# Optimization experiments

Measured on AMD Instinct MI355X. Metric: run time of the kernel, lower is better.

The kernel has to match this reference:

```python
import jax, jax.numpy as jnp
import numpy as np

B, T, H, IN = 256, 1024, 512, 1

def setup_inputs() -> dict:
    key = jax.random.key(0)
    ks = jax.random.split(key, 10)
    s = 1.0 / np.sqrt(H)
    return {
        "input": jax.random.normal(ks[0], (B, T), dtype=jnp.float32),
        "Wx0": jax.random.uniform(ks[1], (IN, 4 * H), jnp.float32, -s, s),
        "Wh0": jax.random.uniform(ks[2], (H, 4 * H), jnp.float32, -s, s),
        "b0": jax.random.uniform(ks[3], (4 * H,), jnp.float32, -s, s),
        "Wx1": jax.random.uniform(ks[4], (H, 4 * H), jnp.float32, -s, s),
        "Wh1": jax.random.uniform(ks[5], (H, 4 * H), jnp.float32, -s, s),
        "b1": jax.random.uniform(ks[6], (4 * H,), jnp.float32, -s, s),
        "Wf": jax.random.uniform(ks[7], (H, 1), jnp.float32, -s, s),
        "bf": jax.random.uniform(ks[8], (1,), jnp.float32, -s, s),
    }

def _lstm_layer(xs, Wx, Wh, b):
    # xs: [T, B, in] -> hs: [T, B, H]
    Bd = xs.shape[1]
    Hd = Wh.shape[0]
    h0 = jnp.zeros((Bd, Hd), xs.dtype)
    c0 = jnp.zeros((Bd, Hd), xs.dtype)
    def step(carry, x_t):
        h, c = carry
        g = x_t @ Wx + h @ Wh + b                     # [B, 4H]
        i, f, gg, o = jnp.split(g, 4, axis=-1)
        i = jax.nn.sigmoid(i)
        f = jax.nn.sigmoid(f)
        gg = jnp.tanh(gg)
        o = jax.nn.sigmoid(o)
        c_n = f * c + i * gg
        h_n = o * jnp.tanh(c_n)
        return (h_n, c_n), h_n
    _, hs = jax.lax.scan(step, (h0, c0), xs)
    return hs

def reference(input, Wx0, Wh0, b0, Wx1, Wh1, b1, Wf, bf):
    # input: [B, T] scalar sequence (input_size = 1)
    xs = input.T[:, :, None]                           # [T, B, 1]
    h1 = _lstm_layer(xs, Wx0, Wh0, b0)                 # [T, B, H]
    h2 = _lstm_layer(h1, Wx1, Wh1, b1)                 # [T, B, H]
    out = h2 @ Wf + bf                                 # [T, B, 1]
    return out[:, :, 0].T                              # [B, T]
```

## Files before the change

### kernel.cpp

```cpp
#include <hip/hip_runtime.h>


typedef _Float16 f16;
typedef _Float16 f16x8 __attribute__((ext_vector_type(8)));
typedef float f32x4 __attribute__((ext_vector_type(4)));
typedef unsigned long long u64;

#define NB 256
#define NT_ 1024
#define NH 512
#define RING 16
#define SLOT (NB * NH)

__device__ __forceinline__ float sigm(float x)  { return 1.0f / (1.0f + __expf(-x)); }
__device__ __forceinline__ float tanhx(float x) { return 2.0f / (1.0f + __expf(-2.0f * x)) - 1.0f; }

__device__ __forceinline__ void st8(unsigned short* p, u64 v) {
  __hip_atomic_store((u64*)p, v, __ATOMIC_RELAXED, __HIP_MEMORY_SCOPE_AGENT);
}
__device__ __forceinline__ void stf(unsigned* p, unsigned v) {
  __hip_atomic_store(p, v, __ATOMIC_RELAXED, __HIP_MEMORY_SCOPE_AGENT);
}
__device__ __forceinline__ unsigned ldf(const unsigned* p) {
  return __hip_atomic_load(p, __ATOMIC_RELAXED, __HIP_MEMORY_SCOPE_AGENT);
}
__device__ __forceinline__ unsigned pollr(const unsigned* a, unsigned thr) {
  unsigned v;
  for (;;) {
    v = ldf(a);
    if (!~__ballot(v >= thr)) break;
    __builtin_amdgcn_s_sleep(1);
  }
  asm volatile("" ::: "memory");
  return v;
}

__device__ __forceinline__ unsigned* PFL(unsigned* pf, int c, int j, int r) {
  return pf + (((c * 32 + j) * 4) + r) * 32;
}
__device__ __forceinline__ unsigned* QFL(unsigned* qf, int c, int j, int r) {
  return qf + (((c * 32 + j) * 4) + r) * 32;
}

__global__ void prep_xT(const float* __restrict__ inp, float* __restrict__ xT) {
  int g = blockIdx.x * 256 + threadIdx.x;
  int t = g >> 8, b = g & 255;
  xT[t * NB + b] = inp[b * NT_ + t];
}

__global__ void prep_w(const float* __restrict__ Wh0,
                       const float* __restrict__ Wx1,
                       const float* __restrict__ Wh1,
                       f16* __restrict__ dst) {
  int g = blockIdx.x * 256 + threadIdx.x;
  int mat = g >> 20;
  int r = g & 0xFFFFF;
  int j = r & 7, ln = (r >> 3) & 63, kt = (r >> 9) & 15;
  int cl = ln & 15, qd = ln >> 4;
  int k = kt * 32 + qd * 8 + j;
  int jt = (r >> 13) & 1, nh = (r >> 14) & 1, sl = (r >> 15) & 31;
  const float* W = (mat == 0) ? Wh0 : (mat == 1) ? Wx1 : Wh1;
  int gate = jt * 2 + (cl >> 3);
  int gcol = gate * 512 + sl * 16 + nh * 8 + (cl & 7);
  size_t di = (size_t)mat * 1048576 + (size_t)sl * 32768 +
              (((size_t)(nh * 2 + jt) * 16 + kt) * 64 + ln) * 8 + j;
  dst[di] = (f16)W[(size_t)k * 2048 + gcol];
}

__global__ void reduce_out(const float* __restrict__ part8,
                           const float* __restrict__ bfp,
                           float* __restrict__ out) {
  int g = blockIdx.x * 256 + threadIdx.x;
  float v = bfp[0];
#pragma unroll
  for (int j = 0; j < 8; ++j) v += part8[(size_t)j * (NB * NT_) + g];
  out[g] = v;
}

__global__ __launch_bounds__(256, 1) void lstm_main(
    const float* __restrict__ xT,
    const f16*  __restrict__ wsl,
    const float* __restrict__ wx0,
    const float* __restrict__ bias0,
    const float* __restrict__ bias1,
    const float* __restrict__ wf,
    unsigned short* p_hi, unsigned short* p_lo,
    unsigned short* q_hi, unsigned short* q_lo,
    unsigned int* pf,
    unsigned int* qf,
    float* part8)
{
  extern __shared__ char smem[];
  const int tid = threadIdx.x;
  const int wv = tid >> 6, ln = tid & 63;
  const int qd = ln >> 4, cl = ln & 15;
  const int bx = blockIdx.x;
  const int r8 = bx & 7, idx = bx >> 3;
  const bool isL0 = !(r8 & 1);
  const int c = r8 >> 1;
  const int sl = idx;
  const float LO = 1.0f / 1024.0f;
  const int u = cl & 7, g01 = cl >> 3;
  const bool hiH = (cl < 8);
  const int lr = wv * 16 + cl;

  if (isL0) {
    const int4* s0 = (const int4*)wsl + (size_t)sl * 4096;
    int4* d = (int4*)smem;
    for (int i = tid; i < 4096; i += 256) d[i] = s0[i];
  } else {
    const int4* s1 = (const int4*)wsl + 131072 + (size_t)sl * 4096;
    const int4* s2 = (const int4*)wsl + 262144 + (size_t)sl * 4096;
    int4* d = (int4*)smem;
    for (int i = tid; i < 4096; i += 256) { d[i] = s1[i]; d[4096 + i] = s2[i]; }
  }
  __syncthreads();

  if (isL0) {
    float w0a[2], w0b[2], b0a[2], b0b[2];
#pragma unroll
    for (int nh = 0; nh < 2; ++nh) {
      int base = sl * 16 + nh * 8 + u;
      w0a[nh] = wx0[g01 * 512 + base];
      b0a[nh] = bias0[g01 * 512 + base];
      w0b[nh] = wx0[(2 + g01) * 512 + base];
      b0b[nh] = bias0[(2 + g01) * 512 + base];
    }
    float cst[2][4] = {{0.f,0.f,0.f,0.f},{0.f,0.f,0.f,0.f}};
    const unsigned* pwa = (ln < 32) ? PFL(pf, c, ln, sl & 3)
                                    : QFL(qf, c, ln - 32, sl & 3);
    const f16x8* wl = (const f16x8*)smem;
    f16* sh  = (f16*)(smem + 65536);
    f16* slo = sh + 1024;

    for (int s = 0; s < NT_; ++s) {
      if ((s & (RING - 1)) == 0 && s) {
        __syncthreads();
        if (wv == 0)
          asm volatile("buffer_inv sc1\n\ts_waitcnt vmcnt(0)" ::: "memory");
        __syncthreads();
      }
      const int slot_r = (s + RING - 1) & (RING - 1);
      const int slot_w = s & (RING - 1);
      float4 xv = *(const float4*)(xT + s * NB + c * 64 + wv * 16 + qd * 4);
      if (s) {
        unsigned thr = (ln < 32) ? (unsigned)s
                                 : (s >= RING ? (unsigned)(s - RING + 1) : 0u);
        pollr(pwa, thr);
      }
      const f16* ah = (const f16*)p_hi + (size_t)slot_r * SLOT + (size_t)c * 32768 +
                      (qd >> 1) * 1024 + lr * 16 + (qd & 1) * 8;
      const f16* al = (const f16*)p_lo + (size_t)slot_r * SLOT + (size_t)c * 32768 +
                      (qd >> 1) * 1024 + lr * 16 + (qd & 1) * 8;
      f16x8 Ah[16], Al[16];
#pragma unroll
      for (int kt = 0; kt < 16; ++kt) {
        Ah[kt] = *(const f16x8*)(ah + kt * 2048);
        Al[kt] = *(const f16x8*)(al + kt * 2048);
      }
      f32x4 acc[4], accL[4];
#pragma unroll
      for (int t4 = 0; t4 < 4; ++t4) {
        acc[t4] = (f32x4){0.f,0.f,0.f,0.f};
        accL[t4] = (f32x4){0.f,0.f,0.f,0.f};
      }
#pragma unroll
      for (int kt = 0; kt < 16; ++kt) {
#pragma unroll
        for (int t4 = 0; t4 < 4; ++t4) {
          f16x8 bw = wl[(t4 * 16 + kt) * 64 + ln];
          acc[t4]  = __builtin_amdgcn_mfma_f32_16x16x32_f16(Ah[kt], bw, acc[t4], 0, 0, 0);
          accL[t4] = __builtin_amdgcn_mfma_f32_16x16x32_f16(Al[kt], bw, accL[t4], 0, 0, 0);
        }
      }
#pragma unroll
      for (int e = 0; e < 4; ++e) {
        float xe = (e == 0) ? xv.x : (e == 1) ? xv.y : (e == 2) ? xv.z : xv.w;
        int r = wv * 16 + qd * 4 + e;
#pragma unroll
        for (int nh = 0; nh < 2; ++nh) {
          float v0 = acc[nh*2+0][e] + accL[nh*2+0][e] * LO + xe * w0a[nh] + b0a[nh];
          float v1 = acc[nh*2+1][e] + accL[nh*2+1][e] * LO + xe * w0b[nh] + b0b[nh];
          float w0 = __shfl_xor(v0, 8, 16);
          float w1 = __shfl_xor(v1, 8, 16);
          float gi = hiH ? v0 : w0;
          float gf = hiH ? w0 : v0;
          float gg = hiH ? v1 : w1;
          float go = hiH ? w1 : v1;
          float ii = sigm(gi), ff = sigm(gf), tg = tanhx(gg), oo = sigm(go);
          cst[nh][e] = ff * cst[nh][e] + ii * tg;
          float h = oo * tanhx(cst[nh][e]);
          int su = r * 16 + nh * 8 + u;
          if (hiH) {
            sh[su] = (f16)h;
          } else {
            f16 hh = (f16)h;
            slo[su] = (f16)((h - (float)hh) * 1024.0f);
          }
        }
      }
      __syncthreads();
      {
        unsigned short* bh = p_hi + (size_t)slot_w * SLOT + (size_t)c * 32768 + (size_t)sl * 1024;
        unsigned short* bl = p_lo + (size_t)slot_w * SLOT + (size_t)c * 32768 + (size_t)sl * 1024;
#pragma unroll
        for (int i = tid; i < 512; i += 256) {
          int strm = i >> 8, pc = i & 255;
          const f16* src = (strm ? slo : sh) + pc * 4;
          st8((strm ? bl : bh) + pc * 4, *(const u64*)src);
        }
      }
      __syncthreads();
      if (tid < 4)
        stf(PFL(pf, c, sl, tid), (unsigned)(s + 1));
    }
  } else {
    float b1c0[2], b1c1[2], wfv[2];
#pragma unroll
    for (int nh = 0; nh < 2; ++nh) {
      int base = sl * 16 + nh * 8 + u;
      b1c0[nh] = bias1[g01 * 512 + base];
      b1c1[nh] = bias1[(2 + g01) * 512 + base];
      wfv[nh] = wf[base];
    }
    float cst[2][4] = {{0.f,0.f,0.f,0.f},{0.f,0.f,0.f,0.f}};
    const unsigned* a_init = (ln < 32) ? QFL(qf, c, ln, sl & 3)
                                       : PFL(pf, c, ln - 32, sl & 3);
    const unsigned* ppf = PFL(pf, c, ln & 31, (sl + (ln >> 5)) & 3);
    const f16x8* wx_ = (const f16x8*)smem;
    const f16x8* wh_ = (const f16x8*)(smem + 65536);
    f16* sh  = (f16*)(smem + 131072);
    f16* slo = sh + 1024;

    for (int s = 0; s < NT_; ++s) {
      if ((s & (RING - 1)) == 0 && s) {
        __syncthreads();
        if (wv == 0)
          asm volatile("buffer_inv sc1\n\ts_waitcnt vmcnt(0)" ::: "memory");
        __syncthreads();
      }
      const int slot_r = (s + RING - 1) & (RING - 1);
      const int slot_w = s & (RING - 1);
      bool early = false;
      if (s) {
        unsigned thr_i = (ln < 32) ? (unsigned)s : (unsigned)(s + 1);
        unsigned v = ldf(a_init);
        u64 bal = __ballot(v >= thr_i);
        while ((unsigned)bal != 0xFFFFFFFFu) {
          __builtin_amdgcn_s_sleep(1);
          v = ldf(a_init);
          bal = __ballot(v >= thr_i);
        }
        asm volatile("" ::: "memory");
        early = ((unsigned)(bal >> 32) == 0xFFFFFFFFu);
      }
      const f16* aqh = (const f16*)q_hi + (size_t)slot_r * SLOT + (size_t)c * 32768 +
                       (qd >> 1) * 1024 + lr * 16 + (qd & 1) * 8;
      const f16* aql = (const f16*)q_lo + (size_t)slot_r * SLOT + (size_t)c * 32768 +
                       (qd >> 1) * 1024 + lr * 16 + (qd & 1) * 8;
      f16x8 Aq[16][2];
#pragma unroll
      for (int kt = 0; kt < 16; ++kt) {
        Aq[kt][0] = *(const f16x8*)(aqh + kt * 2048);
        Aq[kt][1] = *(const f16x8*)(aql + kt * 2048);
      }
      const f16* aph = (const f16*)p_hi + (size_t)slot_w * SLOT + (size_t)c * 32768 +
                       (qd >> 1) * 1024 + lr * 16 + (qd & 1) * 8;
      const f16* apl = (const f16*)p_lo + (size_t)slot_w * SLOT + (size_t)c * 32768 +
                       (qd >> 1) * 1024 + lr * 16 + (qd & 1) * 8;
      f16x8 Ap[16][2];
      if (early) {
#pragma unroll
        for (int kt = 0; kt < 16; ++kt) {
          Ap[kt][0] = *(const f16x8*)(aph + kt * 2048);
          Ap[kt][1] = *(const f16x8*)(apl + kt * 2048);
        }
      }
      f32x4 acc[4], accL[4];
#pragma unroll
      for (int t4 = 0; t4 < 4; ++t4) {
        acc[t4] = (f32x4){0.f,0.f,0.f,0.f};
        accL[t4] = (f32x4){0.f,0.f,0.f,0.f};
      }
#pragma unroll
      for (int kt = 0; kt < 16; ++kt) {
#pragma unroll
        for (int t4 = 0; t4 < 4; ++t4) {
          f16x8 bw = wh_[(t4 * 16 + kt) * 64 + ln];
          acc[t4]  = __builtin_amdgcn_mfma_f32_16x16x32_f16(Aq[kt][0], bw, acc[t4], 0, 0, 0);
          accL[t4] = __builtin_amdgcn_mfma_f32_16x16x32_f16(Aq[kt][1], bw, accL[t4], 0, 0, 0);
        }
      }
      if (!early) {
        pollr(ppf, (unsigned)(s + 1));
#pragma unroll
        for (int kt = 0; kt < 16; ++kt) {
          Ap[kt][0] = *(const f16x8*)(aph + kt * 2048);
          Ap[kt][1] = *(const f16x8*)(apl + kt * 2048);
        }
      }
#pragma unroll
      for (int kt = 0; kt < 16; ++kt) {
#pragma unroll
        for (int t4 = 0; t4 < 4; ++t4) {
          f16x8 bw = wx_[(t4 * 16 + kt) * 64 + ln];
          acc[t4]  = __builtin_amdgcn_mfma_f32_16x16x32_f16(Ap[kt][0], bw, acc[t4], 0, 0, 0);
          accL[t4] = __builtin_amdgcn_mfma_f32_16x16x32_f16(Ap[kt][1], bw, accL[t4], 0, 0, 0);
        }
      }
      float po[4];
#pragma unroll
      for (int e = 0; e < 4; ++e) {
        po[e] = 0.0f;
#pragma unroll
        for (int nh = 0; nh < 2; ++nh) {
          float v0 = acc[nh*2+0][e] + accL[nh*2+0][e] * LO + b1c0[nh];
          float v1 = acc[nh*2+1][e] + accL[nh*2+1][e] * LO + b1c1[nh];
          float w0 = __shfl_xor(v0, 8, 16);
          float w1 = __shfl_xor(v1, 8, 16);
          float gi = hiH ? v0 : w0;
          float gf = hiH ? w0 : v0;
          float gg = hiH ? v1 : w1;
          float go = hiH ? w1 : v1;
          float ii = sigm(gi), ff = sigm(gf), tg = tanhx(gg), oo = sigm(go);
          cst[nh][e] = ff * cst[nh][e] + ii * tg;
          float h = oo * tanhx(cst[nh][e]);
          int su = (wv * 16 + qd * 4 + e) * 16 + nh * 8 + u;
          if (hiH) {
            sh[su] = (f16)h;
          } else {
            f16 hh = (f16)h;
            slo[su] = (f16)((h - (float)hh) * 1024.0f);
          }
          po[e] += hiH ? wfv[nh] * h : 0.0f;
        }
      }
      __syncthreads();
      {
        unsigned short* bhq = q_hi + (size_t)slot_w * SLOT + (size_t)c * 32768 + (size_t)sl * 1024;
        unsigned short* blq = q_lo + (size_t)slot_w * SLOT + (size_t)c * 32768 + (size_t)sl * 1024;
#pragma unroll
        for (int i = tid; i < 512; i += 256) {
          int strm = i >> 8, pc = i & 255;
          const f16* src = (strm ? slo : sh) + pc * 4;
          st8((strm ? blq : bhq) + pc * 4, *(const u64*)src);
        }
      }
      __syncthreads();
      if (tid < 4)
        stf(QFL(qf, c, sl, tid), (unsigned)(s + 1));
#pragma unroll
      for (int e = 0; e < 4; ++e) {
        float r = po[e];
#pragma unroll
        for (int m = 1; m < 16; m <<= 1) r += __shfl_xor(r, m, 16);
        if (cl == 0)
          atomicAdd(part8 + (size_t)(sl & 7) * (NB * NT_) +
                        (size_t)(c * 64 + wv * 16 + qd * 4 + e) * NT_ + s, r);
      }
    }
  }
}

extern "C" void kernel_launch(void* const* d_in, const int* in_sizes, int n_in,
                              void* d_out, int out_size, void* d_ws, size_t ws_size,
                              hipStream_t stream) {
  (void)in_sizes; (void)n_in; (void)out_size; (void)ws_size;
  const float* inp = (const float*)d_in[0];
  const float* Wx0 = (const float*)d_in[1];
  const float* Wh0 = (const float*)d_in[2];
  const float* b0  = (const float*)d_in[3];
  const float* Wx1 = (const float*)d_in[4];
  const float* Wh1 = (const float*)d_in[5];
  const float* b1  = (const float*)d_in[6];
  const float* Wf  = (const float*)d_in[7];
  const float* bf  = (const float*)d_in[8];

  const size_t MB = 1u << 20;
  const size_t OFF_W    = 0;
  const size_t OFF_XT   = 6 * MB;
  const size_t OFF_PHI  = 7 * MB;
  const size_t OFF_PLO  = 11 * MB;
  const size_t OFF_QHI  = 15 * MB;
  const size_t OFF_QLO  = 19 * MB;
  const size_t OFF_PART = 23 * MB;
  const size_t OFF_CTR  = 31 * MB;

  char* ws = (char*)d_ws;
  f16* wsl = (f16*)(ws + OFF_W);
  float* xT = (float*)(ws + OFF_XT);
  unsigned short* phi = (unsigned short*)(ws + OFF_PHI);
  unsigned short* plo = (unsigned short*)(ws + OFF_PLO);
  unsigned short* qhi = (unsigned short*)(ws + OFF_QHI);
  unsigned short* qlo = (unsigned short*)(ws + OFF_QLO);
  float* part8 = (float*)(ws + OFF_PART);
  unsigned int* pfl = (unsigned int*)(ws + OFF_CTR);
  unsigned int* qfl = pfl + 16384;
  float* out = (float*)d_out;

  (void)hipFuncSetAttribute((const void*)lstm_main,
                            hipFuncAttributeMaxDynamicSharedMemorySize, 135168);

  (void)hipMemsetAsync(ws + OFF_PHI, 0, (OFF_CTR + 131072) - OFF_PHI, stream);

  prep_xT<<<1024, 256, 0, stream>>>(inp, xT);
  prep_w<<<12288, 256, 0, stream>>>(Wh0, Wx1, Wh1, wsl);

  lstm_main<<<256, 256, 135168, stream>>>(xT, wsl, Wx0, b0, b1, Wf,
                                          phi, plo, qhi, qlo, pfl, qfl, part8);

  reduce_out<<<1024, 256, 0, stream>>>(part8, bf, out);
}
```

Before: 9.664 ms.

## Add XCC-local fast path for LSTM step exchange with L2-scope sync

At startup each block reads its XCC id. When all 32 blocks of a group share one XCC, the group takes a fast path that exchanges per-step hidden states through XCC-local ring buffers using plain volatile stores and loads, buffer_inv without sc1, and new local flags. Layer-1 blocks copy the layer-0 output from the global ring into a local import buffer, so the cross-layer handoff is decoupled from the local recurrence. The global ring shrinks to 8 slots. The aim is to avoid the cost of device-scope coherence on every recurrent step, at the price of extra copies, more flags, and dependence on the scheduler placing groups on the same XCC.

```diff
diff --git a/kernel.cpp b/kernel.cpp
--- a/kernel.cpp
+++ b/kernel.cpp
@@ -9,7 +9,8 @@
 #define NB 256
 #define NT_ 1024
 #define NH 512
-#define RING 16
+#define RING 8
+#define RL 4
 #define SLOT (NB * NH)
 
 __device__ __forceinline__ float sigm(float x)  { return 1.0f / (1.0f + __expf(-x)); }
@@ -23,6 +24,9 @@
 }
 __device__ __forceinline__ unsigned ldf(const unsigned* p) {
   return __hip_atomic_load(p, __ATOMIC_RELAXED, __HIP_MEMORY_SCOPE_AGENT);
+}
+__device__ __forceinline__ u64 ldf64(const unsigned short* p) {
+  return __hip_atomic_load((const u64*)p, __ATOMIC_RELAXED, __HIP_MEMORY_SCOPE_AGENT);
 }
 __device__ __forceinline__ unsigned pollr(const unsigned* a, unsigned thr) {
   unsigned v;
@@ -34,12 +38,26 @@
   asm volatile("" ::: "memory");
   return v;
 }
+__device__ __forceinline__ void stv32(unsigned* p, unsigned v) { *(volatile unsigned*)p = v; }
+__device__ __forceinline__ void stv64(unsigned short* p, u64 v) { *(volatile u64*)p = v; }
+__device__ __forceinline__ void pollv(const unsigned* a, unsigned thr) {
+  for (;;) {
+    unsigned v = *(volatile const unsigned*)a;
+    if (!~__ballot(v >= thr)) break;
+    __builtin_amdgcn_s_sleep(1);
+    asm volatile("buffer_inv" ::: "memory");
+  }
+  asm volatile("" ::: "memory");
+}
 
 __device__ __forceinline__ unsigned* PFL(unsigned* pf, int c, int j, int r) {
   return pf + (((c * 32 + j) * 4) + r) * 32;
 }
 __device__ __forceinline__ unsigned* QFL(unsigned* qf, int c, int j, int r) {
   return qf + (((c * 32 + j) * 4) + r) * 32;
+}
+__device__ __forceinline__ unsigned* LFL(unsigned* lf, int kind, int c, int j) {
+  return lf + (((kind * 4 + c) * 32) + j) * 32;
 }
 
 __global__ void prep_xT(const float* __restrict__ inp, float* __restrict__ xT) {
@@ -86,8 +104,12 @@
     const float* __restrict__ wf,
     unsigned short* p_hi, unsigned short* p_lo,
     unsigned short* q_hi, unsigned short* q_lo,
-    unsigned int* pf,
-    unsigned int* qf,
+    unsigned int* pf, unsigned int* qf,
+    unsigned short* ploc_hi, unsigned short* ploc_lo,
+    unsigned short* qloc_hi, unsigned short* qloc_lo,
+    unsigned short* pimp_hi, unsigned short* pimp_lo,
+    unsigned int* lf,
+    unsigned int* xtab,
     float* part8)
 {
   extern __shared__ char smem[];
@@ -114,6 +136,13 @@
     int4* d = (int4*)smem;
     for (int i = tid; i < 4096; i += 256) { d[i] = s1[i]; d[4096 + i] = s2[i]; }
   }
+
+  unsigned myx;
+  asm("s_getreg_b32 %0, hwreg(HW_REG_XCC_ID)" : "=s"(myx));
+  unsigned* xgrp = xtab + (isL0 ? 0 : 128) + c * 32;
+  if (tid == 0) stf(xgrp + sl, myx + 1);
+  unsigned xv_ = pollr(xgrp + (ln & 31), 1);
+  bool fast = __all((int)(xv_ == (unsigned)__shfl((int)xv_, 0)));
   __syncthreads();
 
   if (isL0) {
@@ -127,31 +156,54 @@
       b0b[nh] = bias0[(2 + g01) * 512 + base];
     }
     float cst[2][4] = {{0.f,0.f,0.f,0.f},{0.f,0.f,0.f,0.f}};
-    const unsigned* pwa = (ln < 32) ? PFL(pf, c, ln, sl & 3)
-                                    : QFL(qf, c, ln - 32, sl & 3);
     const f16x8* wl = (const f16x8*)smem;
     f16* sh  = (f16*)(smem + 65536);
     f16* slo = sh + 1024;
+    const unsigned* lpf = (const unsigned*)LFL(lf, 0, c, ln & 31);
+    const unsigned* agq = QFL(qf, c, ln & 31, sl & 3);
 
     for (int s = 0; s < NT_; ++s) {
-      if ((s & (RING - 1)) == 0 && s) {
-        __syncthreads();
-        if (wv == 0)
-          asm volatile("buffer_inv sc1\n\ts_waitcnt vmcnt(0)" ::: "memory");
-        __syncthreads();
-      }
-      const int slot_r = (s + RING - 1) & (RING - 1);
-      const int slot_w = s & (RING - 1);
+      const int inv_per = fast ? (RL - 1) : (RING - 1);
+      if ((s & inv_per) == 0 && s) {
+        __syncthreads();
+        if (wv == 0) {
+          if (fast) asm volatile("buffer_inv" ::: "memory");
+          else      asm volatile("buffer_inv sc1\n\ts_waitcnt vmcnt(0)" ::: "memory");
+        }
+        __syncthreads();
+      }
+      const int slw8 = s & (RING - 1);
       float4 xv = *(const float4*)(xT + s * NB + c * 64 + wv * 16 + qd * 4);
       if (s) {
-        unsigned thr = (ln < 32) ? (unsigned)s
-                                 : (s >= RING ? (unsigned)(s - RING + 1) : 0u);
-        pollr(pwa, thr);
-      }
-      const f16* ah = (const f16*)p_hi + (size_t)slot_r * SLOT + (size_t)c * 32768 +
-                      (qd >> 1) * 1024 + lr * 16 + (qd & 1) * 8;
-      const f16* al = (const f16*)p_lo + (size_t)slot_r * SLOT + (size_t)c * 32768 +
-                      (qd >> 1) * 1024 + lr * 16 + (qd & 1) * 8;
+        unsigned thrG = (s >= RING) ? (unsigned)(s - RING + 1) : 0u;
+        if (fast) {
+          for (;;) {
+            unsigned v = (ln < 32) ? *(volatile const unsigned*)lpf : ldf(agq);
+            unsigned t = (ln < 32) ? (unsigned)s : thrG;
+            if (!~__ballot(v >= t)) break;
+            __builtin_amdgcn_s_sleep(1);
+            asm volatile("buffer_inv" ::: "memory");
+          }
+          asm volatile("" ::: "memory");
+        } else {
+          const unsigned* pwa = (ln < 32) ? PFL(pf, c, ln, sl & 3) : agq;
+          pollr(pwa, (ln < 32) ? (unsigned)s : thrG);
+        }
+      }
+      const f16* ah; const f16* al;
+      if (fast) {
+        int slr = (s + RL - 1) & (RL - 1);
+        size_t b0_ = (size_t)(c * RL + slr) * 32768 +
+                     (qd >> 1) * 1024 + lr * 16 + (qd & 1) * 8;
+        ah = (const f16*)ploc_hi + b0_;
+        al = (const f16*)ploc_lo + b0_;
+      } else {
+        int slr8 = (s + RING - 1) & (RING - 1);
+        size_t b0_ = (size_t)slr8 * SLOT + (size_t)c * 32768 +
+                     (qd >> 1) * 1024 + lr * 16 + (qd & 1) * 8;
+        ah = (const f16*)p_hi + b0_;
+        al = (const f16*)p_lo + b0_;
+      }
       f16x8 Ah[16], Al[16];
 #pragma unroll
       for (int kt = 0; kt < 16; ++kt) {
@@ -200,19 +252,48 @@
         }
       }
       __syncthreads();
-      {
-        unsigned short* bh = p_hi + (size_t)slot_w * SLOT + (size_t)c * 32768 + (size_t)sl * 1024;
-        unsigned short* bl = p_lo + (size_t)slot_w * SLOT + (size_t)c * 32768 + (size_t)sl * 1024;
+      if (fast) {
+        if (s && tid < 4) stf(PFL(pf, c, sl, tid), (unsigned)s);
+        {
+          unsigned short* bh = ploc_hi + (size_t)(c * RL + (s & (RL - 1))) * 32768 + (size_t)sl * 1024;
+          unsigned short* bl = ploc_lo + (size_t)(c * RL + (s & (RL - 1))) * 32768 + (size_t)sl * 1024;
+#pragma unroll
+          for (int i = tid; i < 512; i += 256) {
+            int strm = i >> 8, pc = i & 255;
+            const f16* src = (strm ? slo : sh) + pc * 4;
+            stv64((strm ? bl : bh) + pc * 4, *(const u64*)src);
+          }
+        }
+        asm volatile("s_waitcnt vmcnt(0)" ::: "memory");
+        __syncthreads();
+        if (tid == 0) stv32(LFL(lf, 0, c, sl), (unsigned)(s + 1));
+        {
+          unsigned short* bh = p_hi + (size_t)slw8 * SLOT + (size_t)c * 32768 + (size_t)sl * 1024;
+          unsigned short* bl = p_lo + (size_t)slw8 * SLOT + (size_t)c * 32768 + (size_t)sl * 1024;
+#pragma unroll
+          for (int i = tid; i < 512; i += 256) {
+            int strm = i >> 8, pc = i & 255;
+            const f16* src = (strm ? slo : sh) + pc * 4;
+            st8((strm ? bl : bh) + pc * 4, *(const u64*)src);
+          }
+        }
+      } else {
+        unsigned short* bh = p_hi + (size_t)slw8 * SLOT + (size_t)c * 32768 + (size_t)sl * 1024;
+        unsigned short* bl = p_lo + (size_t)slw8 * SLOT + (size_t)c * 32768 + (size_t)sl * 1024;
 #pragma unroll
         for (int i = tid; i < 512; i += 256) {
           int strm = i >> 8, pc = i & 255;
           const f16* src = (strm ? slo : sh) + pc * 4;
           st8((strm ? bl : bh) + pc * 4, *(const u64*)src);
         }
-      }
+        __syncthreads();
+        if (tid < 4) stf(PFL(pf, c, sl, tid), (unsigned)(s + 1));
+      }
+    }
+    if (fast) {
+      asm volatile("s_waitcnt vmcnt(0)" ::: "memory");
       __syncthreads();
-      if (tid < 4)
-        stf(PFL(pf, c, sl, tid), (unsigned)(s + 1));
+      if (tid < 4) stf(PFL(pf, c, sl, tid), (unsigned)NT_);
     }
   } else {
     float b1c0[2], b1c1[2], wfv[2];
@@ -224,139 +305,255 @@
       wfv[nh] = wf[base];
     }
     float cst[2][4] = {{0.f,0.f,0.f,0.f},{0.f,0.f,0.f,0.f}};
-    const unsigned* a_init = (ln < 32) ? QFL(qf, c, ln, sl & 3)
-                                       : PFL(pf, c, ln - 32, sl & 3);
-    const unsigned* ppf = PFL(pf, c, ln & 31, (sl + (ln >> 5)) & 3);
     const f16x8* wx_ = (const f16x8*)smem;
     const f16x8* wh_ = (const f16x8*)(smem + 65536);
     f16* sh  = (f16*)(smem + 131072);
     f16* slo = sh + 1024;
+    const unsigned* lqf = (const unsigned*)LFL(lf, 1, c, ln & 31);
+    const unsigned* lif = (const unsigned*)LFL(lf, 2, c, ln & 31);
 
     for (int s = 0; s < NT_; ++s) {
-      if ((s & (RING - 1)) == 0 && s) {
-        __syncthreads();
-        if (wv == 0)
-          asm volatile("buffer_inv sc1\n\ts_waitcnt vmcnt(0)" ::: "memory");
-        __syncthreads();
-      }
-      const int slot_r = (s + RING - 1) & (RING - 1);
-      const int slot_w = s & (RING - 1);
-      bool early = false;
-      if (s) {
-        unsigned thr_i = (ln < 32) ? (unsigned)s : (unsigned)(s + 1);
-        unsigned v = ldf(a_init);
-        u64 bal = __ballot(v >= thr_i);
-        while ((unsigned)bal != 0xFFFFFFFFu) {
-          __builtin_amdgcn_s_sleep(1);
-          v = ldf(a_init);
-          bal = __ballot(v >= thr_i);
-        }
-        asm volatile("" ::: "memory");
-        early = ((unsigned)(bal >> 32) == 0xFFFFFFFFu);
-      }
-      const f16* aqh = (const f16*)q_hi + (size_t)slot_r * SLOT + (size_t)c * 32768 +
-                       (qd >> 1) * 1024 + lr * 16 + (qd & 1) * 8;
-      const f16* aql = (const f16*)q_lo + (size_t)slot_r * SLOT + (size_t)c * 32768 +
-                       (qd >> 1) * 1024 + lr * 16 + (qd & 1) * 8;
-      f16x8 Aq[16][2];
-#pragma unroll
-      for (int kt = 0; kt < 16; ++kt) {
-        Aq[kt][0] = *(const f16x8*)(aqh + kt * 2048);
-        Aq[kt][1] = *(const f16x8*)(aql + kt * 2048);
-      }
-      const f16* aph = (const f16*)p_hi + (size_t)slot_w * SLOT + (size_t)c * 32768 +
-                       (qd >> 1) * 1024 + lr * 16 + (qd & 1) * 8;
-      const f16* apl = (const f16*)p_lo + (size_t)slot_w * SLOT + (size_t)c * 32768 +
-                       (qd >> 1) * 1024 + lr * 16 + (qd & 1) * 8;
-      f16x8 Ap[16][2];
-      if (early) {
+      const int inv_per = fast ? (RL - 1) : (RING - 1);
+      if ((s & inv_per) == 0 && s) {
+        __syncthreads();
+        if (wv == 0) {
+          if (fast) asm volatile("buffer_inv" ::: "memory");
+          else      asm volatile("buffer_inv sc1\n\ts_waitcnt vmcnt(0)" ::: "memory");
+        }
+        __syncthreads();
+      }
+      const int slw8 = s & (RING - 1);
+      const int slw4 = s & (RL - 1);
+
+      if (fast) {
+        if (s) pollv(lqf, (unsigned)s);
+        pollr(PFL(pf, c, sl, ln & 3), (unsigned)(s + 1));
+        {
+          size_t so = (size_t)slw8 * SLOT + (size_t)c * 32768 + (size_t)sl * 1024 + tid * 4;
+          size_t dof = (size_t)(c * RL + slw4) * 32768 + (size_t)sl * 1024 + tid * 4;
+          u64 vh = ldf64(p_hi + so);
+          u64 vl = ldf64(p_lo + so);
+          stv64(pimp_hi + dof, vh);
+          stv64(pimp_lo + dof, vl);
+        }
+        asm volatile("s_waitcnt vmcnt(0)" ::: "memory");
+        __syncthreads();
+        if (tid == 0) stv32(LFL(lf, 2, c, sl), (unsigned)(s + 1));
+        size_t qb = (size_t)(c * RL + ((s + RL - 1) & (RL - 1))) * 32768 +
+                    (qd >> 1) * 1024 + lr * 16 + (qd & 1) * 8;
+        const f16* aqh = (const f16*)qloc_hi + qb;
+        const f16* aql = (const f16*)qloc_lo + qb;
+        f16x8 Aq[16][2];
+#pragma unroll
+        for (int kt = 0; kt < 16; ++kt) {
+          Aq[kt][0] = *(const f16x8*)(aqh + kt * 2048);
+          Aq[kt][1] = *(const f16x8*)(aql + kt * 2048);
+        }
+        f32x4 acc[4], accL[4];
+#pragma unroll
+        for (int t4 = 0; t4 < 4; ++t4) {
+          acc[t4] = (f32x4){0.f,0.f,0.f,0.f};
+          accL[t4] = (f32x4){0.f,0.f,0.f,0.f};
+        }
+#pragma unroll
+        for (int kt = 0; kt < 16; ++kt) {
+#pragma unroll
+          for (int t4 = 0; t4 < 4; ++t4) {
+            f16x8 bw = wh_[(t4 * 16 + kt) * 64 + ln];
+            acc[t4]  = __builtin_amdgcn_mfma_f32_16x16x32_f16(Aq[kt][0], bw, acc[t4], 0, 0, 0);
+            accL[t4] = __builtin_amdgcn_mfma_f32_16x16x32_f16(Aq[kt][1], bw, accL[t4], 0, 0, 0);
+          }
+        }
+        pollv(lif, (unsigned)(s + 1));
+        size_t pb = (size_t)(c * RL + slw4) * 32768 +
+                    (qd >> 1) * 1024 + lr * 16 + (qd & 1) * 8;
+        const f16* aph = (const f16*)pimp_hi + pb;
+        const f16* apl = (const f16*)pimp_lo + pb;
+        f16x8 Ap[16][2];
 #pragma unroll
         for (int kt = 0; kt < 16; ++kt) {
           Ap[kt][0] = *(const f16x8*)(aph + kt * 2048);
           Ap[kt][1] = *(const f16x8*)(apl + kt * 2048);
         }
-      }
-      f32x4 acc[4], accL[4];
-#pragma unroll
-      for (int t4 = 0; t4 < 4; ++t4) {
-        acc[t4] = (f32x4){0.f,0.f,0.f,0.f};
-        accL[t4] = (f32x4){0.f,0.f,0.f,0.f};
-      }
-#pragma unroll
-      for (int kt = 0; kt < 16; ++kt) {
+#pragma unroll
+        for (int kt = 0; kt < 16; ++kt) {
+#pragma unroll
+          for (int t4 = 0; t4 < 4; ++t4) {
+            f16x8 bw = wx_[(t4 * 16 + kt) * 64 + ln];
+            acc[t4]  = __builtin_amdgcn_mfma_f32_16x16x32_f16(Ap[kt][0], bw, acc[t4], 0, 0, 0);
+            accL[t4] = __builtin_amdgcn_mfma_f32_16x16x32_f16(Ap[kt][1], bw, accL[t4], 0, 0, 0);
+          }
+        }
+        float po[4];
+#pragma unroll
+        for (int e = 0; e < 4; ++e) {
+          po[e] = 0.0f;
+#pragma unroll
+          for (int nh = 0; nh < 2; ++nh) {
+            float v0 = acc[nh*2+0][e] + accL[nh*2+0][e] * LO + b1c0[nh];
+            float v1 = acc[nh*2+1][e] + accL[nh*2+1][e] * LO + b1c1[nh];
+            float w0 = __shfl_xor(v0, 8, 16);
+            float w1 = __shfl_xor(v1, 8, 16);
+            float gi = hiH ? v0 : w0;
+            float gf = hiH ? w0 : v0;
+            float gg = hiH ? v1 : w1;
+            float go = hiH ? w1 : v1;
+            float ii = sigm(gi), ff = sigm(gf), tg = tanhx(gg), oo = sigm(go);
+            cst[nh][e] = ff * cst[nh][e] + ii * tg;
+            float h = oo * tanhx(cst[nh][e]);
+            int su = (wv * 16 + qd * 4 + e) * 16 + nh * 8 + u;
+            if (hiH) {
+              sh[su] = (f16)h;
+            } else {
+              f16 hh = (f16)h;
+              slo[su] = (f16)((h - (float)hh) * 1024.0f);
+            }
+            po[e] += hiH ? wfv[nh] * h : 0.0f;
+          }
+        }
+        __syncthreads();
+        {
+          unsigned short* bh = qloc_hi + (size_t)(c * RL + slw4) * 32768 + (size_t)sl * 1024;
+          unsigned short* bl = qloc_lo + (size_t)(c * RL + slw4) * 32768 + (size_t)sl * 1024;
+#pragma unroll
+          for (int i = tid; i < 512; i += 256) {
+            int strm = i >> 8, pc = i & 255;
+            const f16* src = (strm ? slo : sh) + pc * 4;
+            stv64((strm ? bl : bh) + pc * 4, *(const u64*)src);
+          }
+        }
+        asm volatile("s_waitcnt vmcnt(0)" ::: "memory");
+        __syncthreads();
+        if (tid == 0) stv32(LFL(lf, 1, c, sl), (unsigned)(s + 1));
+        if (tid < 4) stf(QFL(qf, c, sl, tid), (unsigned)(s + 1));
+#pragma unroll
+        for (int e = 0; e < 4; ++e) {
+          float r = po[e];
+#pragma unroll
+          for (int m = 1; m < 16; m <<= 1) r += __shfl_xor(r, m, 16);
+          if (cl == 0)
+            atomicAdd(part8 + (size_t)(sl & 7) * (NB * NT_) +
+                          (size_t)(c * 64 + wv * 16 + qd * 4 + e) * NT_ + s, r);
+        }
+      } else {
+        bool early = false;
+        if (s) {
+          const unsigned* a_init = (ln < 32) ? QFL(qf, c, ln, sl & 3)
+                                             : PFL(pf, c, ln - 32, sl & 3);
+          unsigned thr_i = (ln < 32) ? (unsigned)s : (unsigned)(s + 1);
+          unsigned v = ldf(a_init);
+          u64 bal = __ballot(v >= thr_i);
+          while ((unsigned)bal != 0xFFFFFFFFu) {
+            __builtin_amdgcn_s_sleep(1);
+            v = ldf(a_init);
+            bal = __ballot(v >= thr_i);
+          }
+          asm volatile("" ::: "memory");
+          early = ((unsigned)(bal >> 32) == 0xFFFFFFFFu);
+        }
+        size_t qb = (size_t)((s + RING - 1) & (RING - 1)) * SLOT + (size_t)c * 32768 +
+                    (qd >> 1) * 1024 + lr * 16 + (qd & 1) * 8;
+        const f16* aqh = (const f16*)q_hi + qb;
+        const f16* aql = (const f16*)q_lo + qb;
+        f16x8 Aq[16][2];
+#pragma unroll
+        for (int kt = 0; kt < 16; ++kt) {
+          Aq[kt][0] = *(const f16x8*)(aqh + kt * 2048);
+          Aq[kt][1] = *(const f16x8*)(aql + kt * 2048);
+        }
+        size_t pb = (size_t)slw8 * SLOT + (size_t)c * 32768 +
+                    (qd >> 1) * 1024 + lr * 16 + (qd & 1) * 8;
+        const f16* aph = (const f16*)p_hi + pb;
+        const f16* apl = (const f16*)p_lo + pb;
+        f16x8 Ap[16][2];
+        if (early) {
+#pragma unroll
+          for (int kt = 0; kt < 16; ++kt) {
+            Ap[kt][0] = *(const f16x8*)(aph + kt * 2048);
+            Ap[kt][1] = *(const f16x8*)(apl + kt * 2048);
+          }
+        }
+        f32x4 acc[4], accL[4];
 #pragma unroll
         for (int t4 = 0; t4 < 4; ++t4) {
-          f16x8 bw = wh_[(t4 * 16 + kt) * 64 + ln];
-          acc[t4]  = __builtin_amdgcn_mfma_f32_16x16x32_f16(Aq[kt][0], bw, acc[t4], 0, 0, 0);
-          accL[t4] = __builtin_amdgcn_mfma_f32_16x16x32_f16(Aq[kt][1], bw, accL[t4], 0, 0, 0);
-        }
-      }
-      if (!early) {
-        pollr(ppf, (unsigned)(s + 1));
+          acc[t4] = (f32x4){0.f,0.f,0.f,0.f};
+          accL[t4] = (f32x4){0.f,0.f,0.f,0.f};
+        }
 #pragma unroll
         for (int kt = 0; kt < 16; ++kt) {
-          Ap[kt][0] = *(const f16x8*)(aph + kt * 2048);
-          Ap[kt][1] = *(const f16x8*)(apl + kt * 2048);
-        }
-      }
-#pragma unroll
-      for (int kt = 0; kt < 16; ++kt) {
-#pragma unroll
-        for (int t4 = 0; t4 < 4; ++t4) {
-          f16x8 bw = wx_[(t4 * 16 + kt) * 64 + ln];
-          acc[t4]  = __builtin_amdgcn_mfma_f32_16x16x32_f16(Ap[kt][0], bw, acc[t4], 0, 0, 0);
-          accL[t4] = __builtin_amdgcn_mfma_f32_16x16x32_f16(Ap[kt][1], bw, accL[t4], 0, 0, 0);
-        }
-      }
-      float po[4];
-#pragma unroll
-      for (int e = 0; e < 4; ++e) {
-        po[e] = 0.0f;
-#pragma unroll
-        for (int nh = 0; nh < 2; ++nh) {
-          float v0 = acc[nh*2+0][e] + accL[nh*2+0][e] * LO + b1c0[nh];
-          float v1 = acc[nh*2+1][e] + accL[nh*2+1][e] * LO + b1c1[nh];
-          float w0 = __shfl_xor(v0, 8, 16);
-          float w1 = __shfl_xor(v1, 8, 16);
-          float gi = hiH ? v0 : w0;
-          float gf = hiH ? w0 : v0;
-          float gg = hiH ? v1 : w1;
-          float go = hiH ? w1 : v1;
-          float ii = sigm(gi), ff = sigm(gf), tg = tanhx(gg), oo = sigm(go);
-          cst[nh][e] = ff * cst[nh][e] + ii * tg;
-          float h = oo * tanhx(cst[nh][e]);
-          int su = (wv * 16 + qd * 4 + e) * 16 + nh * 8 + u;
-          if (hiH) {
-            sh[su] = (f16)h;
-          } else {
-            f16 hh = (f16)h;
-            slo[su] = (f16)((h - (float)hh) * 1024.0f);
-          }
-          po[e] += hiH ? wfv[nh] * h : 0.0f;
-        }
-      }
-      __syncthreads();
-      {
-        unsigned short* bhq = q_hi + (size_t)slot_w * SLOT + (size_t)c * 32768 + (size_t)sl * 1024;
-        unsigned short* blq = q_lo + (size_t)slot_w * SLOT + (size_t)c * 32768 + (size_t)sl * 1024;
-#pragma unroll
-        for (int i = tid; i < 512; i += 256) {
-          int strm = i >> 8, pc = i & 255;
-          const f16* src = (strm ? slo : sh) + pc * 4;
-          st8((strm ? blq : bhq) + pc * 4, *(const u64*)src);
-        }
-      }
-      __syncthreads();
-      if (tid < 4)
-        stf(QFL(qf, c, sl, tid), (unsigned)(s + 1));
-#pragma unroll
-      for (int e = 0; e < 4; ++e) {
-        float r = po[e];
-#pragma unroll
-        for (int m = 1; m < 16; m <<= 1) r += __shfl_xor(r, m, 16);
-        if (cl == 0)
-          atomicAdd(part8 + (size_t)(sl & 7) * (NB * NT_) +
-                        (size_t)(c * 64 + wv * 16 + qd * 4 + e) * NT_ + s, r);
+#pragma unroll
+          for (int t4 = 0; t4 < 4; ++t4) {
+            f16x8 bw = wh_[(t4 * 16 + kt) * 64 + ln];
+            acc[t4]  = __builtin_amdgcn_mfma_f32_16x16x32_f16(Aq[kt][0], bw, acc[t4], 0, 0, 0);
+            accL[t4] = __builtin_amdgcn_mfma_f32_16x16x32_f16(Aq[kt][1], bw, accL[t4], 0, 0, 0);
+          }
+        }
+        if (!early) {
+          pollr(PFL(pf, c, ln & 31, (sl + (ln >> 5)) & 3), (unsigned)(s + 1));
+#pragma unroll
+          for (int kt = 0; kt < 16; ++kt) {
+            Ap[kt][0] = *(const f16x8*)(aph + kt * 2048);
+            Ap[kt][1] = *(const f16x8*)(apl + kt * 2048);
+          }
+        }
+#pragma unroll
+        for (int kt = 0; kt < 16; ++kt) {
+#pragma unroll
+          for (int t4 = 0; t4 < 4; ++t4) {
+            f16x8 bw = wx_[(t4 * 16 + kt) * 64 + ln];
+            acc[t4]  = __builtin_amdgcn_mfma_f32_16x16x32_f16(Ap[kt][0], bw, acc[t4], 0, 0, 0);
+            accL[t4] = __builtin_amdgcn_mfma_f32_16x16x32_f16(Ap[kt][1], bw, accL[t4], 0, 0, 0);
+          }
+        }
+        float po[4];
+#pragma unroll
+        for (int e = 0; e < 4; ++e) {
+          po[e] = 0.0f;
+#pragma unroll
+          for (int nh = 0; nh < 2; ++nh) {
+            float v0 = acc[nh*2+0][e] + accL[nh*2+0][e] * LO + b1c0[nh];
+            float v1 = acc[nh*2+1][e] + accL[nh*2+1][e] * LO + b1c1[nh];
+            float w0 = __shfl_xor(v0, 8, 16);
+            float w1 = __shfl_xor(v1, 8, 16);
+            float gi = hiH ? v0 : w0;
+            float gf = hiH ? w0 : v0;
+            float gg = hiH ? v1 : w1;
+            float go = hiH ? w1 : v1;
+            float ii = sigm(gi), ff = sigm(gf), tg = tanhx(gg), oo = sigm(go);
+            cst[nh][e] = ff * cst[nh][e] + ii * tg;
+            float h = oo * tanhx(cst[nh][e]);
+            int su = (wv * 16 + qd * 4 + e) * 16 + nh * 8 + u;
+            if (hiH) {
+              sh[su] = (f16)h;
+            } else {
+              f16 hh = (f16)h;
+              slo[su] = (f16)((h - (float)hh) * 1024.0f);
+            }
+            po[e] += hiH ? wfv[nh] * h : 0.0f;
+          }
+        }
+        __syncthreads();
+        {
+          unsigned short* bhq = q_hi + (size_t)slw8 * SLOT + (size_t)c * 32768 + (size_t)sl * 1024;
+          unsigned short* blq = q_lo + (size_t)slw8 * SLOT + (size_t)c * 32768 + (size_t)sl * 1024;
+#pragma unroll
+          for (int i = tid; i < 512; i += 256) {
+            int strm = i >> 8, pc = i & 255;
+            const f16* src = (strm ? slo : sh) + pc * 4;
+            st8((strm ? blq : bhq) + pc * 4, *(const u64*)src);
+          }
+        }
+        __syncthreads();
+        if (tid < 4) stf(QFL(qf, c, sl, tid), (unsigned)(s + 1));
+#pragma unroll
+        for (int e = 0; e < 4; ++e) {
+          float r = po[e];
+#pragma unroll
+          for (int m = 1; m < 16; m <<= 1) r += __shfl_xor(r, m, 16);
+          if (cl == 0)
+            atomicAdd(part8 + (size_t)(sl & 7) * (NB * NT_) +
+                          (size_t)(c * 64 + wv * 16 + qd * 4 + e) * NT_ + s, r);
+        }
       }
     }
   }
@@ -377,14 +574,23 @@
   const float* bf  = (const float*)d_in[8];
 
   const size_t MB = 1u << 20;
-  const size_t OFF_W    = 0;
-  const size_t OFF_XT   = 6 * MB;
-  const size_t OFF_PHI  = 7 * MB;
-  const size_t OFF_PLO  = 11 * MB;
-  const size_t OFF_QHI  = 15 * MB;
-  const size_t OFF_QLO  = 19 * MB;
-  const size_t OFF_PART = 23 * MB;
-  const size_t OFF_CTR  = 31 * MB;
+  const size_t OFF_W     = 0;
+  const size_t OFF_XT    = 6 * MB;
+  const size_t OFF_PHI   = 7 * MB;
+  const size_t OFF_PLO   = 9 * MB;
+  const size_t OFF_QHI   = 11 * MB;
+  const size_t OFF_QLO   = 13 * MB;
+  const size_t OFF_PART  = 15 * MB;
+  const size_t OFF_PF    = 23 * MB;
+  const size_t OFF_QF    = OFF_PF + 65536;
+  const size_t OFF_XTAB  = OFF_QF + 65536;
+  const size_t OFF_LF    = OFF_XTAB + 4096;
+  const size_t OFF_PLOCH = 24 * MB;
+  const size_t OFF_PLOCL = 25 * MB;
+  const size_t OFF_QLOCH = 26 * MB;
+  const size_t OFF_QLOCL = 27 * MB;
+  const size_t OFF_PIMPH = 28 * MB;
+  const size_t OFF_PIMPL = 29 * MB;
 
   char* ws = (char*)d_ws;
   f16* wsl = (f16*)(ws + OFF_W);
@@ -394,20 +600,30 @@
   unsigned short* qhi = (unsigned short*)(ws + OFF_QHI);
   unsigned short* qlo = (unsigned short*)(ws + OFF_QLO);
   float* part8 = (float*)(ws + OFF_PART);
-  unsigned int* pfl = (unsigned int*)(ws + OFF_CTR);
-  unsigned int* qfl = pfl + 16384;
+  unsigned int* pfl = (unsigned int*)(ws + OFF_PF);
+  unsigned int* qfl = (unsigned int*)(ws + OFF_QF);
+  unsigned int* xtab = (unsigned int*)(ws + OFF_XTAB);
+  unsigned int* lf  = (unsigned int*)(ws + OFF_LF);
+  unsigned short* ploch = (unsigned short*)(ws + OFF_PLOCH);
+  unsigned short* plocl = (unsigned short*)(ws + OFF_PLOCL);
+  unsigned short* qloch = (unsigned short*)(ws + OFF_QLOCH);
+  unsigned short* qlocl = (unsigned short*)(ws + OFF_QLOCL);
+  unsigned short* pimph = (unsigned short*)(ws + OFF_PIMPH);
+  unsigned short* pimpl = (unsigned short*)(ws + OFF_PIMPL);
   float* out = (float*)d_out;
 
   (void)hipFuncSetAttribute((const void*)lstm_main,
                             hipFuncAttributeMaxDynamicSharedMemorySize, 135168);
 
-  (void)hipMemsetAsync(ws + OFF_PHI, 0, (OFF_CTR + 131072) - OFF_PHI, stream);
+  (void)hipMemsetAsync(ws + OFF_PHI, 0, 23 * MB, stream);
 
   prep_xT<<<1024, 256, 0, stream>>>(inp, xT);
   prep_w<<<12288, 256, 0, stream>>>(Wh0, Wx1, Wh1, wsl);
 
   lstm_main<<<256, 256, 135168, stream>>>(xT, wsl, Wx0, b0, b1, Wf,
-                                          phi, plo, qhi, qlo, pfl, qfl, part8);
+                                          phi, plo, qhi, qlo, pfl, qfl,
+                                          ploch, plocl, qloch, qlocl,
+                                          pimph, pimpl, lf, xtab, part8);
 
   reduce_out<<<1024, 256, 0, stream>>>(part8, bf, out);
 }
```

Result: slower. 12.94 ms (+33.9%).

## Split recurrent K loop into halves gated by separate producer flags

Applied to the files above, without the earlier changes.

Each layer's recurrent matmul is split into two K halves. The first half waits only on flags from the first 16 producer slices, and the second half polls the remaining 16 flags after the first half's MFMAs. Layer 0 also defers its check that layer 1 has freed the ring slot until just before it writes its output, instead of checking at step start. The aim is to overlap cross-block synchronisation latency with matrix work on the critical recurrent path, at the cost of more flag polling and more complex ordering.

```diff
diff --git a/kernel.cpp b/kernel.cpp
--- a/kernel.cpp
+++ b/kernel.cpp
@@ -33,6 +33,9 @@
   }
   asm volatile("" ::: "memory");
   return v;
+}
+__device__ __forceinline__ bool chk(unsigned v, unsigned thr) {
+  return !~__ballot(v >= thr);
 }
 
 __device__ __forceinline__ unsigned* PFL(unsigned* pf, int c, int j, int r) {
@@ -127,8 +130,9 @@
       b0b[nh] = bias0[(2 + g01) * 512 + base];
     }
     float cst[2][4] = {{0.f,0.f,0.f,0.f},{0.f,0.f,0.f,0.f}};
-    const unsigned* pwa = (ln < 32) ? PFL(pf, c, ln, sl & 3)
-                                    : QFL(qf, c, ln - 32, sl & 3);
+    const unsigned* pw0 = PFL(pf, c, ln & 15, (sl + (ln >> 4)) & 3);
+    const unsigned* pw1 = PFL(pf, c, 16 + (ln & 15), (sl + (ln >> 4)) & 3);
+    const unsigned* pwg = QFL(qf, c, ln & 31, (sl + (ln >> 5)) & 3);
     const f16x8* wl = (const f16x8*)smem;
     f16* sh  = (f16*)(smem + 65536);
     f16* slo = sh + 1024;
@@ -143,21 +147,19 @@
       const int slot_r = (s + RING - 1) & (RING - 1);
       const int slot_w = s & (RING - 1);
       float4 xv = *(const float4*)(xT + s * NB + c * 64 + wv * 16 + qd * 4);
-      if (s) {
-        unsigned thr = (ln < 32) ? (unsigned)s
-                                 : (s >= RING ? (unsigned)(s - RING + 1) : 0u);
-        pollr(pwa, thr);
-      }
+      if (s) pollr(pw0, (unsigned)s);
       const f16* ah = (const f16*)p_hi + (size_t)slot_r * SLOT + (size_t)c * 32768 +
                       (qd >> 1) * 1024 + lr * 16 + (qd & 1) * 8;
       const f16* al = (const f16*)p_lo + (size_t)slot_r * SLOT + (size_t)c * 32768 +
                       (qd >> 1) * 1024 + lr * 16 + (qd & 1) * 8;
-      f16x8 Ah[16], Al[16];
-#pragma unroll
-      for (int kt = 0; kt < 16; ++kt) {
+      f16x8 Ah[8], Al[8];
+#pragma unroll
+      for (int kt = 0; kt < 8; ++kt) {
         Ah[kt] = *(const f16x8*)(ah + kt * 2048);
         Al[kt] = *(const f16x8*)(al + kt * 2048);
       }
+      unsigned v1 = s ? ldf(pw1) : 0xFFFFFFFFu;
+      unsigned vg = ldf(pwg);
       f32x4 acc[4], accL[4];
 #pragma unroll
       for (int t4 = 0; t4 < 4; ++t4) {
@@ -165,7 +167,7 @@
         accL[t4] = (f32x4){0.f,0.f,0.f,0.f};
       }
 #pragma unroll
-      for (int kt = 0; kt < 16; ++kt) {
+      for (int kt = 0; kt < 8; ++kt) {
 #pragma unroll
         for (int t4 = 0; t4 < 4; ++t4) {
           f16x8 bw = wl[(t4 * 16 + kt) * 64 + ln];
@@ -173,6 +175,23 @@
           accL[t4] = __builtin_amdgcn_mfma_f32_16x16x32_f16(Al[kt], bw, accL[t4], 0, 0, 0);
         }
       }
+      if (s && !chk(v1, (unsigned)s)) pollr(pw1, (unsigned)s);
+      asm volatile("" ::: "memory");
+      f16x8 Bh[8], Bl[8];
+#pragma unroll
+      for (int kt = 0; kt < 8; ++kt) {
+        Bh[kt] = *(const f16x8*)(ah + (kt + 8) * 2048);
+        Bl[kt] = *(const f16x8*)(al + (kt + 8) * 2048);
+      }
+#pragma unroll
+      for (int kt = 0; kt < 8; ++kt) {
+#pragma unroll
+        for (int t4 = 0; t4 < 4; ++t4) {
+          f16x8 bw = wl[(t4 * 16 + (kt + 8)) * 64 + ln];
+          acc[t4]  = __builtin_amdgcn_mfma_f32_16x16x32_f16(Bh[kt], bw, acc[t4], 0, 0, 0);
+          accL[t4] = __builtin_amdgcn_mfma_f32_16x16x32_f16(Bl[kt], bw, accL[t4], 0, 0, 0);
+        }
+      }
 #pragma unroll
       for (int e = 0; e < 4; ++e) {
         float xe = (e == 0) ? xv.x : (e == 1) ? xv.y : (e == 2) ? xv.z : xv.w;
@@ -180,13 +199,13 @@
 #pragma unroll
         for (int nh = 0; nh < 2; ++nh) {
           float v0 = acc[nh*2+0][e] + accL[nh*2+0][e] * LO + xe * w0a[nh] + b0a[nh];
-          float v1 = acc[nh*2+1][e] + accL[nh*2+1][e] * LO + xe * w0b[nh] + b0b[nh];
+          float v1g = acc[nh*2+1][e] + accL[nh*2+1][e] * LO + xe * w0b[nh] + b0b[nh];
           float w0 = __shfl_xor(v0, 8, 16);
-          float w1 = __shfl_xor(v1, 8, 16);
+          float w1 = __shfl_xor(v1g, 8, 16);
           float gi = hiH ? v0 : w0;
           float gf = hiH ? w0 : v0;
-          float gg = hiH ? v1 : w1;
-          float go = hiH ? w1 : v1;
+          float gg = hiH ? v1g : w1;
+          float go = hiH ? w1 : v1g;
           float ii = sigm(gi), ff = sigm(gf), tg = tanhx(gg), oo = sigm(go);
           cst[nh][e] = ff * cst[nh][e] + ii * tg;
           float h = oo * tanhx(cst[nh][e]);
@@ -200,6 +219,9 @@
         }
       }
       __syncthreads();
+      unsigned thrG = (s >= RING) ? (unsigned)(s - RING + 1) : 0u;
+      if (!chk(vg, thrG)) pollr(pwg, thrG);
+      asm volatile("" ::: "memory");
       {
         unsigned short* bh = p_hi + (size_t)slot_w * SLOT + (size_t)c * 32768 + (size_t)sl * 1024;
         unsigned short* bl = p_lo + (size_t)slot_w * SLOT + (size_t)c * 32768 + (size_t)sl * 1024;
@@ -224,9 +246,11 @@
       wfv[nh] = wf[base];
     }
     float cst[2][4] = {{0.f,0.f,0.f,0.f},{0.f,0.f,0.f,0.f}};
-    const unsigned* a_init = (ln < 32) ? QFL(qf, c, ln, sl & 3)
+    const unsigned* a_init = (ln < 16) ? QFL(qf, c, ln, sl & 3)
+                           : (ln < 32) ? QFL(qf, c, ln - 16, (sl + 1) & 3)
                                        : PFL(pf, c, ln - 32, sl & 3);
-    const unsigned* ppf = PFL(pf, c, ln & 31, (sl + (ln >> 5)) & 3);
+    const unsigned* qw1 = QFL(qf, c, 16 + (ln & 15), (sl + (ln >> 4)) & 3);
+    const unsigned* pwA = PFL(pf, c, ln & 31, (sl + (ln >> 5)) & 3);
     const f16x8* wx_ = (const f16x8*)smem;
     const f16x8* wh_ = (const f16x8*)(smem + 65536);
     f16* sh  = (f16*)(smem + 131072);
@@ -258,9 +282,9 @@
                        (qd >> 1) * 1024 + lr * 16 + (qd & 1) * 8;
       const f16* aql = (const f16*)q_lo + (size_t)slot_r * SLOT + (size_t)c * 32768 +
                        (qd >> 1) * 1024 + lr * 16 + (qd & 1) * 8;
-      f16x8 Aq[16][2];
-#pragma unroll
-      for (int kt = 0; kt < 16; ++kt) {
+      f16x8 Aq[8][2];
+#pragma unroll
+      for (int kt = 0; kt < 8; ++kt) {
         Aq[kt][0] = *(const f16x8*)(aqh + kt * 2048);
         Aq[kt][1] = *(const f16x8*)(aql + kt * 2048);
       }
@@ -276,6 +300,7 @@
           Ap[kt][1] = *(const f16x8*)(apl + kt * 2048);
         }
       }
+      unsigned vq1 = s ? ldf(qw1) : 0xFFFFFFFFu;
       f32x4 acc[4], accL[4];
 #pragma unroll
       for (int t4 = 0; t4 < 4; ++t4) {
@@ -283,7 +308,7 @@
         accL[t4] = (f32x4){0.f,0.f,0.f,0.f};
       }
 #pragma unroll
-      for (int kt = 0; kt < 16; ++kt) {
+      for (int kt = 0; kt < 8; ++kt) {
 #pragma unroll
         for (int t4 = 0; t4 < 4; ++t4) {
           f16x8 bw = wh_[(t4 * 16 + kt) * 64 + ln];
@@ -291,8 +316,25 @@
           accL[t4] = __builtin_amdgcn_mfma_f32_16x16x32_f16(Aq[kt][1], bw, accL[t4], 0, 0, 0);
         }
       }
+      if (s && !chk(vq1, (unsigned)s)) pollr(qw1, (unsigned)s);
+      asm volatile("" ::: "memory");
+      f16x8 Bq[8][2];
+#pragma unroll
+      for (int kt = 0; kt < 8; ++kt) {
+        Bq[kt][0] = *(const f16x8*)(aqh + (kt + 8) * 2048);
+        Bq[kt][1] = *(const f16x8*)(aql + (kt + 8) * 2048);
+      }
+#pragma unroll
+      for (int kt = 0; kt < 8; ++kt) {
+#pragma unroll
+        for (int t4 = 0; t4 < 4; ++t4) {
+          f16x8 bw = wh_[(t4 * 16 + (kt + 8)) * 64 + ln];
+          acc[t4]  = __builtin_amdgcn_mfma_f32_16x16x32_f16(Bq[kt][0], bw, acc[t4], 0, 0, 0);
+          accL[t4] = __builtin_amdgcn_mfma_f32_16x16x32_f16(Bq[kt][1], bw, accL[t4], 0, 0, 0);
+        }
+      }
       if (!early) {
-        pollr(ppf, (unsigned)(s + 1));
+        pollr(pwA, (unsigned)(s + 1));
 #pragma unroll
         for (int kt = 0; kt < 16; ++kt) {
           Ap[kt][0] = *(const f16x8*)(aph + kt * 2048);
@@ -315,13 +357,13 @@
 #pragma unroll
         for (int nh = 0; nh < 2; ++nh) {
           float v0 = acc[nh*2+0][e] + accL[nh*2+0][e] * LO + b1c0[nh];
-          float v1 = acc[nh*2+1][e] + accL[nh*2+1][e] * LO + b1c1[nh];
+          float v1g = acc[nh*2+1][e] + accL[nh*2+1][e] * LO + b1c1[nh];
           float w0 = __shfl_xor(v0, 8, 16);
-          float w1 = __shfl_xor(v1, 8, 16);
+          float w1 = __shfl_xor(v1g, 8, 16);
           float gi = hiH ? v0 : w0;
           float gf = hiH ? w0 : v0;
-          float gg = hiH ? v1 : w1;
-          float go = hiH ? w1 : v1;
+          float gg = hiH ? v1g : w1;
+          float go = hiH ? w1 : v1g;
           float ii = sigm(gi), ff = sigm(gf), tg = tanhx(gg), oo = sigm(go);
           cst[nh][e] = ff * cst[nh][e] + ii * tg;
           float h = oo * tanhx(cst[nh][e]);
```

Result: slower. 11.48 ms (+18.7%).
